# Kernel optimization log

Measured on AMD Instinct MI355X. Metric: run time of the kernel, lower is better.

Reference implementation:

```python
import jax, jax.numpy as jnp
import numpy as np


def setup_inputs() -> dict:
    key = jax.random.key(0)
    ks = jax.random.split(key, 6)
    B, T, U = 4, 160, 80
    De, Dd = 640, 640
    inner, vocab = 640, 1024
    return {
        "enc_state": jax.random.normal(ks[0], (B, T, De), jnp.float32),
        "dec_state": jax.random.normal(ks[1], (B, U, Dd), jnp.float32),
        "W1": jax.random.normal(ks[2], (De + Dd, inner), jnp.float32) * (1.0 / np.sqrt(De + Dd)),
        "b1": jax.random.normal(ks[3], (inner,), jnp.float32) * 0.02,
        "W2": jax.random.normal(ks[4], (inner, vocab), jnp.float32) * (1.0 / np.sqrt(inner)),
        "b2": jax.random.normal(ks[5], (vocab,), jnp.float32) * 0.02,
    }


def reference(enc_state, dec_state, W1, b1, W2, b2):
    # Faithful to: cat([enc tiled over U, dec tiled over T], -1) @ W1 + b1,
    # algebraically split so the [B,T,U,2D] concat is never materialized:
    # cat(e, d) @ W1 == e @ W1[:De] + d @ W1[De:]
    De = enc_state.shape[-1]
    W1_enc, W1_dec = W1[:De], W1[De:]
    enc_proj = jnp.einsum("btd,dh->bth", enc_state, W1_enc)   # [B,T,H]
    dec_proj = jnp.einsum("bud,dh->buh", dec_state, W1_dec)   # [B,U,H]
    # broadcast add over the (T,U) lattice -> [B,T,U,H]
    hidden = jnp.tanh(enc_proj[:, :, None, :] + dec_proj[:, None, :, :] + b1)
    logits = jnp.einsum("btuh,hv->btuv", hidden, W2) + b2     # [B,T,U,V]
    return logits
```

## Files before the change

### kernel.cpp

```cpp
#include <hip/hip_runtime.h>
#include <hip/hip_bf16.h>
#include <cstdint>

#define B_    4
#define T_    160
#define U_    80
#define D_    640
#define V_    1024
#define BT_   640
#define BU_   320
#define M_    51200

typedef __bf16 bf16x8 __attribute__((ext_vector_type(8)));
typedef float floatx4 __attribute__((ext_vector_type(4)));

__device__ __forceinline__ void g2l16(const void* g, void* l) {
    __builtin_amdgcn_global_load_lds((const __attribute__((address_space(1))) void*)g,
                                     (__attribute__((address_space(3))) void*)l,
                                     16, 0, 0);
}

__device__ __forceinline__ float fast_tanh(float x) {
    float e = __builtin_amdgcn_exp2f(x * 2.8853900817779268f);
    return 1.0f - 2.0f * __builtin_amdgcn_rcpf(e + 1.0f);
}

__global__ __launch_bounds__(256) void proj_kernel(
    const float* __restrict__ enc, const float* __restrict__ dec,
    const float* __restrict__ W1,
    float* __restrict__ encp, float* __restrict__ decp) {
    __shared__ float As[32][36];
    __shared__ float Ws[32][36];

    const int rt = blockIdx.y;
    const int ct = blockIdx.x;
    const float* Asrc;
    const float* Wsrc;
    float* Cdst;
    if (rt < 20) { Asrc = enc + (size_t)rt * 32 * D_;        Wsrc = W1;             Cdst = encp + (size_t)rt * 32 * D_; }
    else         { Asrc = dec + (size_t)(rt - 20) * 32 * D_; Wsrc = W1 + D_ * D_;   Cdst = decp + (size_t)(rt - 20) * 32 * D_; }

    const int tid = threadIdx.x;
    const int ar = tid >> 3, ac = (tid & 7) * 4;
    const int tr = tid >> 4, tc = tid & 15;

    float a00 = 0.f, a01 = 0.f, a10 = 0.f, a11 = 0.f;
    for (int k0 = 0; k0 < D_; k0 += 32) {
        __syncthreads();
        *(floatx4*)&As[ar][ac] = *(const floatx4*)&Asrc[(size_t)ar * D_ + k0 + ac];
        *(floatx4*)&Ws[ar][ac] = *(const floatx4*)&Wsrc[(size_t)(k0 + ar) * D_ + ct * 32 + ac];
        __syncthreads();
#pragma unroll
        for (int kk = 0; kk < 32; kk++) {
            float x0 = As[tr * 2][kk], x1 = As[tr * 2 + 1][kk];
            float w0 = Ws[kk][tc * 2], w1 = Ws[kk][tc * 2 + 1];
            a00 += x0 * w0; a01 += x0 * w1;
            a10 += x1 * w0; a11 += x1 * w1;
        }
    }
    const int cc = ct * 32 + tc * 2;
    Cdst[(size_t)(tr * 2) * D_ + cc]     = a00;
    Cdst[(size_t)(tr * 2) * D_ + cc + 1] = a01;
    Cdst[(size_t)(tr * 2 + 1) * D_ + cc]     = a10;
    Cdst[(size_t)(tr * 2 + 1) * D_ + cc + 1] = a11;
}

__global__ __launch_bounds__(256) void w2t_kernel(
    const float* __restrict__ W2, __bf16* __restrict__ W2t) {
    __shared__ __bf16 tile[32][33];
    const int vt = blockIdx.x;
    const int kt = blockIdx.y;
    const int tx = threadIdx.x & 31, ty = threadIdx.x >> 5;
#pragma unroll
    for (int i = 0; i < 4; i++)
        tile[ty + i * 8][tx] = (__bf16)W2[(size_t)(kt * 32 + ty + i * 8) * V_ + vt * 32 + tx];
    __syncthreads();
#pragma unroll
    for (int i = 0; i < 4; i++)
        W2t[(size_t)(vt * 32 + ty + i * 8) * D_ + kt * 32 + tx] = tile[tx][ty + i * 8];
}

__global__ __launch_bounds__(256) void hidden_kernel(
    const float* __restrict__ encp, const float* __restrict__ decp,
    const float* __restrict__ b1, __bf16* __restrict__ H) {
    const unsigned g = blockIdx.x * 256u + threadIdx.x;
    const unsigned row = g / 80u;
    const unsigned hg  = g % 80u;
    const unsigned u   = row % 80u;
    const unsigned bt  = row / 80u;
    const unsigned b   = bt / 160u;

    const float* ep = encp + (size_t)bt * D_ + hg * 8;
    const float* dp = decp + (size_t)(b * 80u + u) * D_ + hg * 8;
    const float* bp = b1 + hg * 8;

    floatx4 e0 = *(const floatx4*)ep,       e1 = *(const floatx4*)(ep + 4);
    floatx4 d0 = *(const floatx4*)dp,       d1 = *(const floatx4*)(dp + 4);
    floatx4 c0 = *(const floatx4*)bp,       c1 = *(const floatx4*)(bp + 4);

    bf16x8 hv;
#pragma unroll
    for (int i = 0; i < 4; i++) hv[i]     = (__bf16)fast_tanh(e0[i] + d0[i] + c0[i]);
#pragma unroll
    for (int i = 0; i < 4; i++) hv[i + 4] = (__bf16)fast_tanh(e1[i] + d1[i] + c1[i]);

    *(bf16x8*)(H + (size_t)g * 8) = hv;
}

__global__ __launch_bounds__(256) void gemm_kernel(
    const __bf16* __restrict__ H, const __bf16* __restrict__ W2t,
    const float* __restrict__ b2, float* __restrict__ C) {
    __shared__ __bf16 As[128 * 32];
    __shared__ __bf16 Bs[128 * 32];

    const int bx = blockIdx.x;
    const int nt = bx & 7;
    const int mt = bx >> 3;
    const int m0 = mt * 128, n0 = nt * 128;

    const int tid = threadIdx.x;
    const int lane = tid & 63;
    const int wave = tid >> 6;
    const int wm = (wave & 1) * 64, wn = (wave >> 1) * 64;
    const int lr = lane & 15, qd = lane >> 4;

    const int r = tid >> 2;
    const int c = (tid & 3) * 8;
    const __bf16* Ag = H   + (size_t)(m0 + r) * D_ + c;
    const __bf16* Bg = W2t + (size_t)(n0 + r) * D_ + c;
    __bf16* Al = &As[r * 32 + c];
    __bf16* Bl = &Bs[r * 32 + c];

    floatx4 acc[4][4] = {};

    for (int k0 = 0; k0 < D_; k0 += 32) {
        __syncthreads();
        g2l16(Ag + k0,                 Al);
        g2l16(Ag + k0 + 64 * D_,       Al + 64 * 32);
        g2l16(Bg + k0,                 Bl);
        g2l16(Bg + k0 + 64 * D_,       Bl + 64 * 32);
        __syncthreads();

        bf16x8 af[4], wf[4];
#pragma unroll
        for (int i = 0; i < 4; i++)
            af[i] = *(const bf16x8*)&As[(wm + i * 16 + lr) * 32 + qd * 8];
#pragma unroll
        for (int j = 0; j < 4; j++)
            wf[j] = *(const bf16x8*)&Bs[(wn + j * 16 + lr) * 32 + qd * 8];
#pragma unroll
        for (int i = 0; i < 4; i++)
#pragma unroll
            for (int j = 0; j < 4; j++)
                acc[i][j] = __builtin_amdgcn_mfma_f32_16x16x32_bf16(af[i], wf[j], acc[i][j], 0, 0, 0);
    }

    float bias[4];
#pragma unroll
    for (int j = 0; j < 4; j++) bias[j] = b2[n0 + wn + j * 16 + lr];
#pragma unroll
    for (int i = 0; i < 4; i++) {
#pragma unroll
        for (int j = 0; j < 4; j++) {
            const int col = n0 + wn + j * 16 + lr;
#pragma unroll
            for (int rg = 0; rg < 4; rg++) {
                const int row = m0 + wm + i * 16 + qd * 4 + rg;
                C[(size_t)row * V_ + col] = acc[i][j][rg] + bias[j];
            }
        }
    }
}

extern "C" void kernel_launch(void* const* d_in, const int* in_sizes, int n_in,
                              void* d_out, int out_size, void* d_ws, size_t ws_size,
                              hipStream_t stream) {
    const float* enc = (const float*)d_in[0];
    const float* dec = (const float*)d_in[1];
    const float* W1  = (const float*)d_in[2];
    const float* b1  = (const float*)d_in[3];
    const float* W2  = (const float*)d_in[4];
    const float* b2  = (const float*)d_in[5];
    float* out = (float*)d_out;

    char* ws = (char*)d_ws;
    float*  encp = (float*)ws;
    float*  decp = (float*)(ws + 1638400);
    __bf16* W2t  = (__bf16*)(ws + 1638400 + 819200);
    __bf16* Hbuf = (__bf16*)(ws + 1638400 + 819200 + 1310720);

    proj_kernel<<<dim3(20, 30), 256, 0, stream>>>(enc, dec, W1, encp, decp);
    w2t_kernel<<<dim3(32, 20), 256, 0, stream>>>(W2, W2t);
    hidden_kernel<<<16000, 256, 0, stream>>>(encp, decp, b1, Hbuf);
    gemm_kernel<<<3200, 256, 0, stream>>>(Hbuf, W2t, b2, out);
}
```

Baseline: 354.6 us.

## Move projection GEMM to bf16 MFMA and vectorize output GEMM stores

Replaces the scalar fp32 projection kernel with a bf16 MFMA GEMM, fed by a new conversion kernel that casts enc/dec to bf16 and transposes W1 and W2. The W2 transpose is merged into that same conversion kernel. The output GEMM swaps its MFMA operand order so each lane holds four consecutive columns, which allows 16-byte vectorized stores of logits plus bias. This targets the slow scalar projection and the dominant scattered 4-byte output writes. The cost is an extra conversion pass and bf16 rounding of the projection inputs.

```diff
diff --git a/kernel.cpp b/kernel.cpp
--- a/kernel.cpp
+++ b/kernel.cpp
@@ -2,13 +2,8 @@
 #include <hip/hip_bf16.h>
 #include <cstdint>
 
-#define B_    4
-#define T_    160
-#define U_    80
 #define D_    640
 #define V_    1024
-#define BT_   640
-#define BU_   320
 #define M_    51200
 
 typedef __bf16 bf16x8 __attribute__((ext_vector_type(8)));
@@ -25,59 +20,115 @@
     return 1.0f - 2.0f * __builtin_amdgcn_rcpf(e + 1.0f);
 }
 
-__global__ __launch_bounds__(256) void proj_kernel(
+__global__ __launch_bounds__(256) void convert_kernel(
     const float* __restrict__ enc, const float* __restrict__ dec,
-    const float* __restrict__ W1,
+    const float* __restrict__ W1, const float* __restrict__ W2,
+    __bf16* __restrict__ enc_b, __bf16* __restrict__ dec_b,
+    __bf16* __restrict__ W1t_enc, __bf16* __restrict__ W1t_dec,
+    __bf16* __restrict__ W2t) {
+    __shared__ __bf16 tile[32][33];
+    const int bid = blockIdx.x;
+    const int tid = threadIdx.x;
+
+    if (bid < 320) {
+        bf16x8 o;
+        if (bid < 200) {
+            const size_t g = (size_t)bid * 2048 + (size_t)tid * 8;
+            floatx4 a = *(const floatx4*)(enc + g);
+            floatx4 b = *(const floatx4*)(enc + g + 4);
+#pragma unroll
+            for (int i = 0; i < 4; i++) { o[i] = (__bf16)a[i]; o[i + 4] = (__bf16)b[i]; }
+            *(bf16x8*)(enc_b + g) = o;
+        } else {
+            const size_t g = (size_t)(bid - 200) * 2048 + (size_t)tid * 8;
+            const unsigned row = (unsigned)(g / 640u);
+            if (row < 320u) {
+                floatx4 a = *(const floatx4*)(dec + g);
+                floatx4 b = *(const floatx4*)(dec + g + 4);
+#pragma unroll
+                for (int i = 0; i < 4; i++) { o[i] = (__bf16)a[i]; o[i + 4] = (__bf16)b[i]; }
+            } else {
+#pragma unroll
+                for (int i = 0; i < 8; i++) o[i] = (__bf16)0.0f;
+            }
+            *(bf16x8*)(dec_b + g) = o;
+        }
+        return;
+    }
+
+    const float* src; __bf16* dst; int nld, tn, tk;
+    if (bid < 720)       { int t = bid - 320;  src = W1;             dst = W1t_enc; nld = 640;  tn = t % 20; tk = t / 20; }
+    else if (bid < 1120) { int t = bid - 720;  src = W1 + 640 * 640; dst = W1t_dec; nld = 640;  tn = t % 20; tk = t / 20; }
+    else                 { int t = bid - 1120; src = W2;             dst = W2t;     nld = 1024; tn = t % 32; tk = t / 32; }
+    const int tx = tid & 31, ty = tid >> 5;
+#pragma unroll
+    for (int i = 0; i < 4; i++)
+        tile[ty + i * 8][tx] = (__bf16)src[(size_t)(tk * 32 + ty + i * 8) * nld + tn * 32 + tx];
+    __syncthreads();
+#pragma unroll
+    for (int i = 0; i < 4; i++)
+        dst[(size_t)(tn * 32 + ty + i * 8) * D_ + tk * 32 + tx] = tile[tx][ty + i * 8];
+}
+
+__global__ __launch_bounds__(256) void proj_gemm_kernel(
+    const __bf16* __restrict__ enc_b, const __bf16* __restrict__ dec_b,
+    const __bf16* __restrict__ W1t_enc, const __bf16* __restrict__ W1t_dec,
     float* __restrict__ encp, float* __restrict__ decp) {
-    __shared__ float As[32][36];
-    __shared__ float Ws[32][36];
-
-    const int rt = blockIdx.y;
-    const int ct = blockIdx.x;
-    const float* Asrc;
-    const float* Wsrc;
-    float* Cdst;
-    if (rt < 20) { Asrc = enc + (size_t)rt * 32 * D_;        Wsrc = W1;             Cdst = encp + (size_t)rt * 32 * D_; }
-    else         { Asrc = dec + (size_t)(rt - 20) * 32 * D_; Wsrc = W1 + D_ * D_;   Cdst = decp + (size_t)(rt - 20) * 32 * D_; }
+    __shared__ __bf16 As[128 * 32];
+    __shared__ __bf16 Bs[128 * 32];
+
+    const int nt = blockIdx.x;
+    const int mt = blockIdx.y;
+    const bool is_enc = (mt < 5);
+    const __bf16* Abase = is_enc ? enc_b + (size_t)mt * 128 * D_
+                                 : dec_b + (size_t)(mt - 5) * 128 * D_;
+    const __bf16* Bbase = (is_enc ? W1t_enc : W1t_dec) + (size_t)nt * 128 * D_;
 
     const int tid = threadIdx.x;
-    const int ar = tid >> 3, ac = (tid & 7) * 4;
-    const int tr = tid >> 4, tc = tid & 15;
-
-    float a00 = 0.f, a01 = 0.f, a10 = 0.f, a11 = 0.f;
+    const int lane = tid & 63;
+    const int wave = tid >> 6;
+    const int wm = (wave & 1) * 64, wn = (wave >> 1) * 64;
+    const int lr = lane & 15, qd = lane >> 4;
+
+    const int r = tid >> 2;
+    const int c = (tid & 3) * 8;
+    const __bf16* Ag = Abase + (size_t)r * D_ + c;
+    const __bf16* Bg = Bbase + (size_t)r * D_ + c;
+    __bf16* Al = &As[r * 32 + c];
+    __bf16* Bl = &Bs[r * 32 + c];
+
+    floatx4 acc[4][4] = {};
     for (int k0 = 0; k0 < D_; k0 += 32) {
         __syncthreads();
-        *(floatx4*)&As[ar][ac] = *(const floatx4*)&Asrc[(size_t)ar * D_ + k0 + ac];
-        *(floatx4*)&Ws[ar][ac] = *(const floatx4*)&Wsrc[(size_t)(k0 + ar) * D_ + ct * 32 + ac];
-        __syncthreads();
-#pragma unroll
-        for (int kk = 0; kk < 32; kk++) {
-            float x0 = As[tr * 2][kk], x1 = As[tr * 2 + 1][kk];
-            float w0 = Ws[kk][tc * 2], w1 = Ws[kk][tc * 2 + 1];
-            a00 += x0 * w0; a01 += x0 * w1;
-            a10 += x1 * w0; a11 += x1 * w1;
+        g2l16(Ag + k0,            Al);
+        g2l16(Ag + k0 + 64 * D_,  Al + 64 * 32);
+        g2l16(Bg + k0,            Bl);
+        g2l16(Bg + k0 + 64 * D_,  Bl + 64 * 32);
+        __syncthreads();
+
+        bf16x8 af[4], wf[4];
+#pragma unroll
+        for (int i = 0; i < 4; i++) af[i] = *(const bf16x8*)&As[(wm + i * 16 + lr) * 32 + qd * 8];
+#pragma unroll
+        for (int j = 0; j < 4; j++) wf[j] = *(const bf16x8*)&Bs[(wn + j * 16 + lr) * 32 + qd * 8];
+#pragma unroll
+        for (int i = 0; i < 4; i++)
+#pragma unroll
+            for (int j = 0; j < 4; j++)
+                acc[i][j] = __builtin_amdgcn_mfma_f32_16x16x32_bf16(wf[j], af[i], acc[i][j], 0, 0, 0);
+    }
+
+    float* Cb = is_enc ? encp + (size_t)mt * 128 * D_ : decp + (size_t)(mt - 5) * 128 * D_;
+    const int rowlim = is_enc ? 128 : 320 - (mt - 5) * 128;
+#pragma unroll
+    for (int i = 0; i < 4; i++) {
+        const int rl = wm + i * 16 + lr;
+        if (rl < rowlim) {
+#pragma unroll
+            for (int j = 0; j < 4; j++)
+                *(floatx4*)&Cb[(size_t)rl * D_ + nt * 128 + wn + j * 16 + qd * 4] = acc[i][j];
         }
     }
-    const int cc = ct * 32 + tc * 2;
-    Cdst[(size_t)(tr * 2) * D_ + cc]     = a00;
-    Cdst[(size_t)(tr * 2) * D_ + cc + 1] = a01;
-    Cdst[(size_t)(tr * 2 + 1) * D_ + cc]     = a10;
-    Cdst[(size_t)(tr * 2 + 1) * D_ + cc + 1] = a11;
-}
-
-__global__ __launch_bounds__(256) void w2t_kernel(
-    const float* __restrict__ W2, __bf16* __restrict__ W2t) {
-    __shared__ __bf16 tile[32][33];
-    const int vt = blockIdx.x;
-    const int kt = blockIdx.y;
-    const int tx = threadIdx.x & 31, ty = threadIdx.x >> 5;
-#pragma unroll
-    for (int i = 0; i < 4; i++)
-        tile[ty + i * 8][tx] = (__bf16)W2[(size_t)(kt * 32 + ty + i * 8) * V_ + vt * 32 + tx];
-    __syncthreads();
-#pragma unroll
-    for (int i = 0; i < 4; i++)
-        W2t[(size_t)(vt * 32 + ty + i * 8) * D_ + kt * 32 + tx] = tile[tx][ty + i * 8];
 }
 
 __global__ __launch_bounds__(256) void hidden_kernel(
@@ -94,9 +145,9 @@
     const float* dp = decp + (size_t)(b * 80u + u) * D_ + hg * 8;
     const float* bp = b1 + hg * 8;
 
-    floatx4 e0 = *(const floatx4*)ep,       e1 = *(const floatx4*)(ep + 4);
-    floatx4 d0 = *(const floatx4*)dp,       d1 = *(const floatx4*)(dp + 4);
-    floatx4 c0 = *(const floatx4*)bp,       c1 = *(const floatx4*)(bp + 4);
+    floatx4 e0 = *(const floatx4*)ep, e1 = *(const floatx4*)(ep + 4);
+    floatx4 d0 = *(const floatx4*)dp, d1 = *(const floatx4*)(dp + 4);
+    floatx4 c0 = *(const floatx4*)bp, c1 = *(const floatx4*)(bp + 4);
 
     bf16x8 hv;
 #pragma unroll
@@ -135,39 +186,31 @@
 
     for (int k0 = 0; k0 < D_; k0 += 32) {
         __syncthreads();
-        g2l16(Ag + k0,                 Al);
-        g2l16(Ag + k0 + 64 * D_,       Al + 64 * 32);
-        g2l16(Bg + k0,                 Bl);
-        g2l16(Bg + k0 + 64 * D_,       Bl + 64 * 32);
+        g2l16(Ag + k0,            Al);
+        g2l16(Ag + k0 + 64 * D_,  Al + 64 * 32);
+        g2l16(Bg + k0,            Bl);
+        g2l16(Bg + k0 + 64 * D_,  Bl + 64 * 32);
         __syncthreads();
 
         bf16x8 af[4], wf[4];
 #pragma unroll
+        for (int i = 0; i < 4; i++) af[i] = *(const bf16x8*)&As[(wm + i * 16 + lr) * 32 + qd * 8];
+#pragma unroll
+        for (int j = 0; j < 4; j++) wf[j] = *(const bf16x8*)&Bs[(wn + j * 16 + lr) * 32 + qd * 8];
+#pragma unroll
         for (int i = 0; i < 4; i++)
-            af[i] = *(const bf16x8*)&As[(wm + i * 16 + lr) * 32 + qd * 8];
-#pragma unroll
-        for (int j = 0; j < 4; j++)
-            wf[j] = *(const bf16x8*)&Bs[(wn + j * 16 + lr) * 32 + qd * 8];
-#pragma unroll
-        for (int i = 0; i < 4; i++)
 #pragma unroll
             for (int j = 0; j < 4; j++)
-                acc[i][j] = __builtin_amdgcn_mfma_f32_16x16x32_bf16(af[i], wf[j], acc[i][j], 0, 0, 0);
-    }
-
-    float bias[4];
-#pragma unroll
-    for (int j = 0; j < 4; j++) bias[j] = b2[n0 + wn + j * 16 + lr];
-#pragma unroll
-    for (int i = 0; i < 4; i++) {
-#pragma unroll
-        for (int j = 0; j < 4; j++) {
-            const int col = n0 + wn + j * 16 + lr;
-#pragma unroll
-            for (int rg = 0; rg < 4; rg++) {
-                const int row = m0 + wm + i * 16 + qd * 4 + rg;
-                C[(size_t)row * V_ + col] = acc[i][j][rg] + bias[j];
-            }
+                acc[i][j] = __builtin_amdgcn_mfma_f32_16x16x32_bf16(wf[j], af[i], acc[i][j], 0, 0, 0);
+    }
+
+#pragma unroll
+    for (int j = 0; j < 4; j++) {
+        const floatx4 bj = *(const floatx4*)&b2[n0 + wn + j * 16 + qd * 4];
+#pragma unroll
+        for (int i = 0; i < 4; i++) {
+            floatx4 v = acc[i][j] + bj;
+            *(floatx4*)&C[(size_t)(m0 + wm + i * 16 + lr) * V_ + n0 + wn + j * 16 + qd * 4] = v;
         }
     }
 }
@@ -184,13 +227,19 @@
     float* out = (float*)d_out;
 
     char* ws = (char*)d_ws;
-    float*  encp = (float*)ws;
-    float*  decp = (float*)(ws + 1638400);
-    __bf16* W2t  = (__bf16*)(ws + 1638400 + 819200);
-    __bf16* Hbuf = (__bf16*)(ws + 1638400 + 819200 + 1310720);
-
-    proj_kernel<<<dim3(20, 30), 256, 0, stream>>>(enc, dec, W1, encp, decp);
-    w2t_kernel<<<dim3(32, 20), 256, 0, stream>>>(W2, W2t);
+    float*  encp    = (float*)ws;
+    float*  decp    = (float*)(ws + 1638400);
+    __bf16* W2t     = (__bf16*)(ws + 2457600);
+    __bf16* Hbuf    = (__bf16*)(ws + 3768320);
+    __bf16* enc_b   = (__bf16*)(ws + 3768320);
+    __bf16* dec_b   = (__bf16*)(ws + 4587520);
+    __bf16* W1t_enc = (__bf16*)(ws + 5079040);
+    __bf16* W1t_dec = (__bf16*)(ws + 5898240);
+
+    convert_kernel<<<1760, 256, 0, stream>>>(enc, dec, W1, W2,
+                                             enc_b, dec_b, W1t_enc, W1t_dec, W2t);
+    proj_gemm_kernel<<<dim3(5, 8), 256, 0, stream>>>(enc_b, dec_b, W1t_enc, W1t_dec,
+                                                     encp, decp);
     hidden_kernel<<<16000, 256, 0, stream>>>(encp, decp, b1, Hbuf);
     gemm_kernel<<<3200, 256, 0, stream>>>(Hbuf, W2t, b2, out);
 }
```

Measured after the change: 357.9 us. About the same (+0.9%).
